# Performance work log

Measured on AMD Instinct MI355X. Metric: run time of the kernel, lower is better.

Reference implementation:

```python
import jax, jax.numpy as jnp
import numpy as np
import math

EMB_DIM = 1024
N_HEADS = 16
HEAD_DIM = EMB_DIM // N_HEADS
B, T = 4, 2048


def bitlinear(x, w):
    # BitNet b1.58 absmean ternary quantization. NOTE: the source never
    # rescales the ternary weights by `scale`, so forward uses raw {-1,0,1}.
    scale = jnp.maximum(jnp.mean(jnp.abs(w)), 1e-8)
    w_ternary = jnp.clip(jnp.round(w / scale), -1.0, 1.0)
    w_q = w + jax.lax.stop_gradient(w_ternary - w)  # STE
    return x @ w_q.T


def setup_inputs() -> dict:
    key = jax.random.key(0)
    k1, k2, k3 = jax.random.split(key, 3)
    x = jax.random.normal(k1, (B, T, EMB_DIM), dtype=jnp.float32)
    w_qkv = jax.random.normal(k2, (3 * EMB_DIM, EMB_DIM), dtype=jnp.float32) * 0.02
    w_out = jax.random.normal(k3, (EMB_DIM, EMB_DIM), dtype=jnp.float32) * 0.02
    return {"x": x, "w_qkv": w_qkv, "w_out": w_out}


def reference(x, w_qkv, w_out):
    Bc, Tc, C = x.shape
    qkv = bitlinear(x, w_qkv)  # [B, T, 3C]
    q, k, v = jnp.split(qkv, 3, axis=2)

    def split_heads(t):  # [B, T, C] -> [B, H, T, D]
        return t.reshape(Bc, Tc, N_HEADS, HEAD_DIM).transpose(0, 2, 1, 3)

    q, k, v = split_heads(q), split_heads(k), split_heads(v)
    scale = math.sqrt(HEAD_DIM)
    scores = jnp.einsum("bhqd,bhkd->bhqk", q, k) / scale  # [B, H, T, T]
    causal = jnp.triu(jnp.ones((Tc, Tc), dtype=bool), k=1)
    scores = jnp.where(causal, -jnp.inf, scores)
    attn = jax.nn.softmax(scores, axis=-1)
    out = jnp.einsum("bhqk,bhkd->bhqd", attn, v)  # [B, H, T, D]
    out = out.transpose(0, 2, 1, 3).reshape(Bc, Tc, C)
    return bitlinear(out, w_out)
```

## Files before the change

### kernel.cpp

```cpp
#include <hip/hip_runtime.h>
#include <hip/hip_bf16.h>

#define EMB   1024
#define NHEAD 16
#define HDIM  64
#define BSZ   4
#define SEQ   2048
#define MROWS (BSZ*SEQ)
#define NQKV  (3*EMB)

typedef __bf16 bf16;
typedef __bf16 bf16v8 __attribute__((ext_vector_type(8)));
typedef float  f32v4  __attribute__((ext_vector_type(4)));
typedef int    i32v4  __attribute__((ext_vector_type(4)));

#define MFMA16(a,b,c)  __builtin_amdgcn_mfma_f32_16x16x32_bf16((a),(b),(c),0,0,0)
#define MFMAI8(a,b,c)  __builtin_amdgcn_mfma_i32_16x16x64_i8((a),(b),(c),0,0,0)

__device__ __forceinline__ void gload_lds16(const void* g, void* l) {
  __builtin_amdgcn_global_load_lds((const __attribute__((address_space(1))) void*)g,
                                   (__attribute__((address_space(3))) void*)l,
                                   16, 0, 0);
}

#define DPP_FMAX(x, ctrl) do {                                                     \
    int _t = __builtin_amdgcn_update_dpp(0, __float_as_int(x), (ctrl), 0xf, 0xf, true); \
    (x) = fmaxf((x), __int_as_float(_t)); } while (0)


__global__ void zero2_kernel(float* p) { p[threadIdx.x] = 0.f; }

__global__ void abs_sum_kernel(const float* __restrict__ w, int n, float* out) {
  float s = 0.f;
  for (int i = blockIdx.x * blockDim.x + threadIdx.x; i < n; i += gridDim.x * blockDim.x)
    s += fabsf(w[i]);
  #pragma unroll
  for (int off = 32; off; off >>= 1) s += __shfl_down(s, off, 64);
  __shared__ float red[4];
  int lane = threadIdx.x & 63, wid = threadIdx.x >> 6;
  if (lane == 0) red[wid] = s;
  __syncthreads();
  if (threadIdx.x == 0) atomicAdd(out, red[0] + red[1] + red[2] + red[3]);
}

__global__ void ternarize_i8_kernel(const float* __restrict__ w, int n,
                                    const float* __restrict__ sum, char* __restrict__ out) {
  int i = blockIdx.x * blockDim.x + threadIdx.x;
  if (i >= n) return;
  float scale = fmaxf(*sum / (float)n, 1e-8f);
  float t = rintf(w[i] / scale);
  t = fmaxf(-1.f, fminf(1.f, t));
  out[i] = (char)(int)t;
}

__global__ void ternarize_bf16_kernel(const float* __restrict__ w, int n,
                                      const float* __restrict__ sum, bf16* __restrict__ out) {
  int i = blockIdx.x * blockDim.x + threadIdx.x;
  if (i >= n) return;
  float scale = fmaxf(*sum / (float)n, 1e-8f);
  float t = rintf(w[i] / scale);
  t = fmaxf(-1.f, fminf(1.f, t));
  out[i] = (bf16)t;
}

__global__ void quant_x_kernel(const float* __restrict__ x, char* __restrict__ p1,
                               char* __restrict__ p2, int n) {
  int i = blockIdx.x * blockDim.x + threadIdx.x;
  if (i >= n) return;
  float v = x[i];
  float q1 = fminf(fmaxf(rintf(v * 16.f), -127.f), 127.f);
  float r = v - q1 * 0.0625f;
  float q2 = fminf(fmaxf(rintf(r * 4096.f), -127.f), 127.f);
  p1[i] = (char)(int)q1;
  p2[i] = (char)(int)q2;
}


__launch_bounds__(256, 2)
__global__ void gemm_qkv_kernel(const char* __restrict__ xq1, const char* __restrict__ xq2,
                                const char* __restrict__ w8,
                                bf16* __restrict__ qh, bf16* __restrict__ ql,
                                bf16* __restrict__ kh, bf16* __restrict__ kl,
                                bf16* __restrict__ vv) {
  __shared__ __align__(16) char A1[128 * 64];
  __shared__ __align__(16) char A2[128 * 64];
  __shared__ __align__(16) char Bs[128 * 64];
  const int tid = threadIdx.x;
  const int lane = tid & 63, wid = tid >> 6;
  const int quad = lane >> 4, l16 = lane & 15;
  const int m0 = blockIdx.x * 128, n0 = blockIdx.y * 128;
  const int wm = (wid >> 1) * 64, wn = (wid & 1) * 64;
  const int asw = (l16 >> 1) & 3;
  i32v4 acc1[4][4] = {};
  i32v4 acc2[4][4] = {};

  for (int kt = 0; kt < EMB / 64; ++kt) {
    __syncthreads();
    #pragma unroll
    for (int r = 0; r < 2; ++r) {
      int li = r * 256 + tid;
      int row = li >> 2, cs = li & 3;
      int cg = cs ^ ((row >> 1) & 3);
      gload_lds16(xq1 + (size_t)(m0 + row) * EMB + kt * 64 + cg * 16, &A1[li * 16]);
      gload_lds16(xq2 + (size_t)(m0 + row) * EMB + kt * 64 + cg * 16, &A2[li * 16]);
      gload_lds16(w8  + (size_t)(n0 + row) * EMB + kt * 64 + cg * 16, &Bs[li * 16]);
    }
    __syncthreads();
    i32v4 af1[4], af2[4], bfr[4];
    #pragma unroll
    for (int i = 0; i < 4; ++i) {
      int arow = wm + i * 16 + l16;
      int off = arow * 64 + ((quad ^ asw) * 16);
      af1[i] = *(const i32v4*)&A1[off];
      af2[i] = *(const i32v4*)&A2[off];
      int brow = wn + i * 16 + l16;
      bfr[i] = *(const i32v4*)&Bs[brow * 64 + ((quad ^ asw) * 16)];
    }
    #pragma unroll
    for (int i = 0; i < 4; ++i)
      #pragma unroll
      for (int j = 0; j < 4; ++j) {
        acc1[i][j] = MFMAI8(af1[i], bfr[j], acc1[i][j]);
        acc2[i][j] = MFMAI8(af2[i], bfr[j], acc2[i][j]);
      }
  }
  const float S1 = 0.0625f, S2 = 1.f / 4096.f;
  const float QSCALE = 0.18033688011112042f;
  #pragma unroll
  for (int i = 0; i < 4; ++i)
    #pragma unroll
    for (int j = 0; j < 4; ++j)
      #pragma unroll
      for (int r = 0; r < 4; ++r) {
        int m = m0 + wm + i * 16 + quad * 4 + r;
        int n = n0 + wn + j * 16 + l16;
        float c = (float)acc1[i][j][r] * S1 + (float)acc2[i][j][r] * S2;
        int b = m >> 11, t = m & (SEQ - 1);
        int region = n >> 10, c1 = n & 1023, h = c1 >> 6, d = c1 & 63;
        size_t idx = (((size_t)(b * NHEAD + h) * SEQ + t) << 6) + d;
        if (region == 0)      { float cs = c * QSCALE; bf16 hi = (bf16)cs; qh[idx] = hi; ql[idx] = (bf16)(cs - (float)hi); }
        else if (region == 1) { bf16 hi = (bf16)c; kh[idx] = hi; kl[idx] = (bf16)(c - (float)hi); }
        else                  { vv[idx] = (bf16)c; }
      }
}


__global__ void transpose_v_kernel(const bf16* __restrict__ v, bf16* __restrict__ vt) {
  __shared__ bf16 tile[64 * 72];
  const int tid = threadIdx.x;
  const int bh = blockIdx.y, t0 = blockIdx.x * 64;
  const size_t base = (size_t)bh * SEQ * HDIM;
  #pragma unroll
  for (int r = 0; r < 2; ++r) {
    int li = r * 256 + tid;
    int row = li >> 3, col = (li & 7) * 8;
    bf16v8 val = *(const bf16v8*)(v + base + (size_t)(t0 + row) * HDIM + col);
    #pragma unroll
    for (int j = 0; j < 8; ++j) tile[(col + j) * 72 + row] = val[j];
  }
  __syncthreads();
  #pragma unroll
  for (int r = 0; r < 2; ++r) {
    int li = r * 256 + tid;
    int drow = li >> 3, tcol = (li & 7) * 8;
    bf16v8 val;
    #pragma unroll
    for (int j = 0; j < 8; ++j) val[j] = tile[drow * 72 + tcol + j];
    *(bf16v8*)(vt + base + (size_t)drow * SEQ + t0 + tcol) = val;
  }
}


__launch_bounds__(256, 2)
__global__ void attn_kernel(const bf16* __restrict__ qh, const bf16* __restrict__ ql,
                            const bf16* __restrict__ kh, const bf16* __restrict__ kl,
                            const bf16* __restrict__ vt, bf16* __restrict__ o) {
  __shared__ __align__(16) char smem[66560];
  bf16* Qh = (bf16*)smem;
  bf16* Ql = (bf16*)(smem + 16384);
  bf16* Pw = (bf16*)(smem + 49152);
  const int tid = threadIdx.x;
  const int lane = tid & 63, wid = tid >> 6;
  const int quad = lane >> 4, l16 = lane & 15;
  const int xs = l16 & 7;
  const int pair = blockIdx.x;
  const int bh = blockIdx.y;
  const size_t base = (size_t)bh * SEQ * HDIM;

  auto stage_kv = [&](char* dst, int k0) {
    #pragma unroll
    for (int r = 0; r < 2; ++r) {
      int li = r * 256 + tid;
      int srow = li >> 3, scg = (li & 7) ^ (srow & 7);
      gload_lds16(kh + base + (size_t)(k0 + srow) * HDIM + scg * 8, (bf16*)dst + (size_t)li * 8);
      gload_lds16(kl + base + (size_t)(k0 + srow) * HDIM + scg * 8, (bf16*)(dst + 8192) + (size_t)li * 8);
      gload_lds16(vt + base + (size_t)srow * SEQ + k0 + scg * 8,    (bf16*)(dst + 16384) + (size_t)li * 8);
    }
  };

  bf16v8 ones_f;
  {
    bf16 v1 = (l16 == 0) ? (bf16)1.0f : (bf16)0.0f;
    #pragma unroll
    for (int j = 0; j < 8; ++j) ones_f[j] = v1;
  }
  const int b = bh >> 4, h = bh & 15;

  for (int phase = 0; phase < 2; ++phase) {
    const int qt = phase ? (7 - pair) : (8 + pair);
    const int q0 = qt * 128;

    __syncthreads();
    #pragma unroll
    for (int r = 0; r < 4; ++r) {
      int li = r * 256 + tid;
      int row = li >> 3, cg = (li & 7) ^ (row & 7);
      gload_lds16(qh + base + (size_t)(q0 + row) * HDIM + cg * 8, &Qh[li * 8]);
      gload_lds16(ql + base + (size_t)(q0 + row) * HDIM + cg * 8, &Ql[li * 8]);
    }
    __syncthreads();
    bf16v8 qhf[2][2], qlf[2][2];
    #pragma unroll
    for (int sub = 0; sub < 2; ++sub)
      #pragma unroll
      for (int kk = 0; kk < 2; ++kk) {
        int off = (wid * 32 + sub * 16 + l16) * 64 + (((kk << 2) | quad) ^ xs) * 8;
        qhf[sub][kk] = *(const bf16v8*)&Qh[off];
        qlf[sub][kk] = *(const bf16v8*)&Ql[off];
      }
    __syncthreads();

    f32v4 oacc[2][4] = {};
    f32v4 lacc[2] = {};
    float mrow[2][4];
    #pragma unroll
    for (int s = 0; s < 2; ++s)
      #pragma unroll
      for (int r = 0; r < 4; ++r) mrow[s][r] = -1e30f;

    const int qw0 = q0 + wid * 32;
    const int qrow_hi = qw0 + 31;
    const int ntiles = 2 * qt + 2;

    stage_kv(smem, 0);

    for (int ktile = 0; ktile < ntiles; ++ktile) {
      char* cb = smem + (size_t)((ktile & 1) * 24576);
      char* nb = smem + (size_t)(((ktile + 1) & 1) * 24576);
      __syncthreads();
      if (ktile + 1 < ntiles) stage_kv(nb, (ktile + 1) * 64);
      const int k0 = ktile * 64;
      if (k0 > qrow_hi) continue;

      bf16* Kh_ = (bf16*)cb;
      bf16* Kl_ = (bf16*)(cb + 8192);
      bf16* Vt_ = (bf16*)(cb + 16384);

      f32v4 sacc[2][4] = {};
      #pragma unroll
      for (int kk = 0; kk < 2; ++kk) {
        const int co = (((kk << 2) | quad) ^ xs) * 8;
        bf16v8 khf[4], klf[4];
        #pragma unroll
        for (int nt = 0; nt < 4; ++nt) {
          khf[nt] = *(const bf16v8*)&Kh_[(nt * 16 + l16) * 64 + co];
          klf[nt] = *(const bf16v8*)&Kl_[(nt * 16 + l16) * 64 + co];
        }
        #pragma unroll
        for (int sub = 0; sub < 2; ++sub)
          #pragma unroll
          for (int nt = 0; nt < 4; ++nt) {
            sacc[sub][nt] = MFMA16(qhf[sub][kk], khf[nt], sacc[sub][nt]);
            sacc[sub][nt] = MFMA16(qhf[sub][kk], klf[nt], sacc[sub][nt]);
            sacc[sub][nt] = MFMA16(qlf[sub][kk], khf[nt], sacc[sub][nt]);
          }
      }

      #pragma unroll
      for (int sub = 0; sub < 2; ++sub) {
        if (k0 > qw0 + sub * 16 + 15) continue;
        const int qrow_base = qw0 + sub * 16 + quad * 4;
        #pragma unroll
        for (int nt = 0; nt < 4; ++nt) {
          int key = k0 + nt * 16 + l16;
          #pragma unroll
          for (int r = 0; r < 4; ++r)
            if (key > qrow_base + r) sacc[sub][nt][r] = -1e30f;
        }
        float alpha[4];
        #pragma unroll
        for (int r = 0; r < 4; ++r) {
          float mx = fmaxf(fmaxf(sacc[sub][0][r], sacc[sub][1][r]),
                           fmaxf(sacc[sub][2][r], sacc[sub][3][r]));
          DPP_FMAX(mx, 0x128);
          DPP_FMAX(mx, 0x124);
          DPP_FMAX(mx, 0x122);
          DPP_FMAX(mx, 0x121);
          float mnew = fmaxf(mrow[sub][r], mx);
          alpha[r] = __builtin_amdgcn_exp2f(mrow[sub][r] - mnew);
          mrow[sub][r] = mnew;
        }
        bf16* pwave = Pw + (wid * 2 + sub) * (16 * 68);
        #pragma unroll
        for (int nt = 0; nt < 4; ++nt)
          #pragma unroll
          for (int r = 0; r < 4; ++r)
            pwave[(quad * 4 + r) * 68 + nt * 16 + l16] =
                (bf16)__builtin_amdgcn_exp2f(sacc[sub][nt][r] - mrow[sub][r]);
        #pragma unroll
        for (int r = 0; r < 4; ++r) {
          lacc[sub][r] *= alpha[r];
          #pragma unroll
          for (int dt = 0; dt < 4; ++dt) oacc[sub][dt][r] *= alpha[r];
        }
      }

      #pragma unroll
      for (int kk = 0; kk < 2; ++kk) {
        const int co = (((kk << 2) | quad) ^ xs) * 8;
        bf16v8 vf[4];
        #pragma unroll
        for (int dt = 0; dt < 4; ++dt)
          vf[dt] = *(const bf16v8*)&Vt_[(dt * 16 + l16) * 64 + co];
        #pragma unroll
        for (int sub = 0; sub < 2; ++sub) {
          if (k0 > qw0 + sub * 16 + 15) continue;
          bf16v8 pf = *(const bf16v8*)&Pw[(wid * 2 + sub) * (16 * 68) + l16 * 68 + kk * 32 + quad * 8];
          lacc[sub] = MFMA16(pf, ones_f, lacc[sub]);
          #pragma unroll
          for (int dt = 0; dt < 4; ++dt)
            oacc[sub][dt] = MFMA16(pf, vf[dt], oacc[sub][dt]);
        }
      }
    }

    #pragma unroll
    for (int sub = 0; sub < 2; ++sub) {
      float lrow[4];
      #pragma unroll
      for (int r = 0; r < 4; ++r) lrow[r] = __shfl(lacc[sub][r], lane & 48, 64);
      #pragma unroll
      for (int dt = 0; dt < 4; ++dt)
        #pragma unroll
        for (int r = 0; r < 4; ++r) {
          int q = q0 + wid * 32 + sub * 16 + quad * 4 + r;
          int d = dt * 16 + l16;
          float val = oacc[sub][dt][r] / lrow[r];
          o[((size_t)(b * SEQ + q)) * EMB + h * HDIM + d] = (bf16)val;
        }
    }
  }
}


__launch_bounds__(256, 2)
__global__ void gemm_out_kernel(const bf16* __restrict__ oin, const bf16* __restrict__ wt,
                                float* __restrict__ out) {
  __shared__ __align__(16) bf16 As_[128 * 64];
  __shared__ __align__(16) bf16 Bs_[128 * 64];
  const int tid = threadIdx.x;
  const int lane = tid & 63, wid = tid >> 6;
  const int quad = lane >> 4, l16 = lane & 15;
  const int m0 = blockIdx.x * 128, n0 = blockIdx.y * 128;
  const int wm = (wid >> 1) * 64, wn = (wid & 1) * 64;
  f32v4 acc[4][4] = {};

  for (int kt = 0; kt < EMB / 64; ++kt) {
    __syncthreads();
    #pragma unroll
    for (int r = 0; r < 4; ++r) {
      int li = r * 256 + tid;
      int row = li >> 3, col = (li & 7) * 8;
      gload_lds16(oin + (size_t)(m0 + row) * EMB + kt * 64 + col, &As_[li * 8]);
      gload_lds16(wt  + (size_t)(n0 + row) * EMB + kt * 64 + col, &Bs_[li * 8]);
    }
    __syncthreads();
    #pragma unroll
    for (int kk = 0; kk < 2; ++kk) {
      bf16v8 af[4], bfr[4];
      #pragma unroll
      for (int i = 0; i < 4; ++i) {
        af[i]  = *(const bf16v8*)&As_[(wm + i * 16 + l16) * 64 + kk * 32 + quad * 8];
        bfr[i] = *(const bf16v8*)&Bs_[(wn + i * 16 + l16) * 64 + kk * 32 + quad * 8];
      }
      #pragma unroll
      for (int i = 0; i < 4; ++i)
        #pragma unroll
        for (int j = 0; j < 4; ++j)
          acc[i][j] = MFMA16(af[i], bfr[j], acc[i][j]);
    }
  }
  #pragma unroll
  for (int i = 0; i < 4; ++i)
    #pragma unroll
    for (int j = 0; j < 4; ++j)
      #pragma unroll
      for (int r = 0; r < 4; ++r) {
        int m = m0 + wm + i * 16 + quad * 4 + r;
        int n = n0 + wn + j * 16 + l16;
        out[(size_t)m * EMB + n] = acc[i][j][r];
      }
}


extern "C" void kernel_launch(void* const* d_in, const int* in_sizes, int n_in,
                              void* d_out, int out_size, void* d_ws, size_t ws_size,
                              hipStream_t stream) {
  const float* x     = (const float*)d_in[0];
  const float* w_qkv = (const float*)d_in[1];
  const float* w_out = (const float*)d_in[2];
  float* out = (float*)d_out;
  char* ws = (char*)d_ws;

  const size_t SZ  = (size_t)MROWS * EMB * sizeof(bf16);
  const size_t SZ8 = (size_t)MROWS * EMB;
  size_t off = 0;
  float* sums = (float*)ws;            off = 256;
  char*  wq8  = (char*)(ws + off);     off += (size_t)NQKV * EMB;
  bf16*  wo_t = (bf16*)(ws + off);     off += (size_t)EMB * EMB * sizeof(bf16);
  char*  xq1  = (char*)(ws + off);     off += SZ8;
  char*  xq2  = (char*)(ws + off);     off += SZ8;
  bf16*  qh   = (bf16*)(ws + off);     off += SZ;
  bf16*  ql   = (bf16*)(ws + off);     off += SZ;
  bf16*  kh   = (bf16*)(ws + off);     off += SZ;
  bf16*  kl   = (bf16*)(ws + off);     off += SZ;
  bf16*  vv   = (bf16*)(ws + off);     off += SZ;
  bf16*  vt   = (bf16*)xq1;
  bf16*  ob   = vv;
  (void)in_sizes; (void)n_in; (void)out_size; (void)ws_size;

  zero2_kernel<<<1, 2, 0, stream>>>(sums);
  abs_sum_kernel<<<256, 256, 0, stream>>>(w_qkv, NQKV * EMB, &sums[0]);
  abs_sum_kernel<<<256, 256, 0, stream>>>(w_out, EMB * EMB, &sums[1]);
  ternarize_i8_kernel<<<(NQKV * EMB) / 256, 256, 0, stream>>>(w_qkv, NQKV * EMB, &sums[0], wq8);
  ternarize_bf16_kernel<<<(EMB * EMB) / 256, 256, 0, stream>>>(w_out, EMB * EMB, &sums[1], wo_t);
  quant_x_kernel<<<(MROWS * EMB) / 256, 256, 0, stream>>>(x, xq1, xq2, MROWS * EMB);
  gemm_qkv_kernel<<<dim3(MROWS / 128, NQKV / 128), 256, 0, stream>>>(xq1, xq2, wq8, qh, ql, kh, kl, vv);
  transpose_v_kernel<<<dim3(SEQ / 64, BSZ * NHEAD), 256, 0, stream>>>(vv, vt);
  attn_kernel<<<dim3(8, BSZ * NHEAD), 256, 0, stream>>>(qh, ql, kh, kl, vt, ob);
  gemm_out_kernel<<<dim3(MROWS / 128, EMB / 128), 256, 0, stream>>>(ob, wo_t, out);
}
```

Measured before the change: 344.6 us.

## Transpose QK^T MFMA so rows map to lanes and simplify online softmax

Swaps the MFMA operand order for scores so each lane owns one query row, which turns the row max and sum into cross-quad shuffles instead of DPP reductions. The row sum is now computed in registers, replacing the ones-vector MFMA. The oacc rescale is skipped when no row max grows. The P buffer is shared per wave instead of per sub-tile, and the sub-0 score MFMAs are skipped when that sub-tile is fully masked. This cuts MFMA and VALU work in the softmax, at the cost of more shuffles and a serialized P write/read per sub-tile.

```diff
diff --git a/kernel.cpp b/kernel.cpp
--- a/kernel.cpp
+++ b/kernel.cpp
@@ -10,6 +10,7 @@
 #define NQKV  (3*EMB)
 
 typedef __bf16 bf16;
+typedef __bf16 bf16v4 __attribute__((ext_vector_type(4)));
 typedef __bf16 bf16v8 __attribute__((ext_vector_type(8)));
 typedef float  f32v4  __attribute__((ext_vector_type(4)));
 typedef int    i32v4  __attribute__((ext_vector_type(4)));
@@ -22,10 +23,6 @@
                                    (__attribute__((address_space(3))) void*)l,
                                    16, 0, 0);
 }
-
-#define DPP_FMAX(x, ctrl) do {                                                     \
-    int _t = __builtin_amdgcn_update_dpp(0, __float_as_int(x), (ctrl), 0xf, 0xf, true); \
-    (x) = fmaxf((x), __int_as_float(_t)); } while (0)
 
 
 __global__ void zero2_kernel(float* p) { p[threadIdx.x] = 0.f; }
@@ -175,7 +172,7 @@
 __global__ void attn_kernel(const bf16* __restrict__ qh, const bf16* __restrict__ ql,
                             const bf16* __restrict__ kh, const bf16* __restrict__ kl,
                             const bf16* __restrict__ vt, bf16* __restrict__ o) {
-  __shared__ __align__(16) char smem[66560];
+  __shared__ __align__(16) char smem[57856];
   bf16* Qh = (bf16*)smem;
   bf16* Ql = (bf16*)(smem + 16384);
   bf16* Pw = (bf16*)(smem + 49152);
@@ -198,13 +195,8 @@
     }
   };
 
-  bf16v8 ones_f;
-  {
-    bf16 v1 = (l16 == 0) ? (bf16)1.0f : (bf16)0.0f;
-    #pragma unroll
-    for (int j = 0; j < 8; ++j) ones_f[j] = v1;
-  }
   const int b = bh >> 4, h = bh & 15;
+  bf16* Ps = Pw + wid * (16 * 68);
 
   for (int phase = 0; phase < 2; ++phase) {
     const int qt = phase ? (7 - pair) : (8 + pair);
@@ -231,12 +223,8 @@
     __syncthreads();
 
     f32v4 oacc[2][4] = {};
-    f32v4 lacc[2] = {};
-    float mrow[2][4];
-    #pragma unroll
-    for (int s = 0; s < 2; ++s)
-      #pragma unroll
-      for (int r = 0; r < 4; ++r) mrow[s][r] = -1e30f;
+    float lsum[2] = {0.f, 0.f};
+    float mrow[2] = {-1e30f, -1e30f};
 
     const int qw0 = q0 + wid * 32;
     const int qrow_hi = qw0 + 31;
@@ -256,6 +244,8 @@
       bf16* Kl_ = (bf16*)(cb + 8192);
       bf16* Vt_ = (bf16*)(cb + 16384);
 
+      const bool live0 = (k0 <= qw0 + 15);
+
       f32v4 sacc[2][4] = {};
       #pragma unroll
       for (int kk = 0; kk < 2; ++kk) {
@@ -267,69 +257,87 @@
           klf[nt] = *(const bf16v8*)&Kl_[(nt * 16 + l16) * 64 + co];
         }
         #pragma unroll
-        for (int sub = 0; sub < 2; ++sub)
+        for (int sub = 0; sub < 2; ++sub) {
+          if (sub == 0 && !live0) continue;
           #pragma unroll
           for (int nt = 0; nt < 4; ++nt) {
-            sacc[sub][nt] = MFMA16(qhf[sub][kk], khf[nt], sacc[sub][nt]);
-            sacc[sub][nt] = MFMA16(qhf[sub][kk], klf[nt], sacc[sub][nt]);
-            sacc[sub][nt] = MFMA16(qlf[sub][kk], khf[nt], sacc[sub][nt]);
+            sacc[sub][nt] = MFMA16(khf[nt], qhf[sub][kk], sacc[sub][nt]);
+            sacc[sub][nt] = MFMA16(klf[nt], qhf[sub][kk], sacc[sub][nt]);
+            sacc[sub][nt] = MFMA16(khf[nt], qlf[sub][kk], sacc[sub][nt]);
           }
+        }
       }
 
       #pragma unroll
       for (int sub = 0; sub < 2; ++sub) {
-        if (k0 > qw0 + sub * 16 + 15) continue;
-        const int qrow_base = qw0 + sub * 16 + quad * 4;
+        if (sub == 0 && !live0) continue;
+        const int dq = (qw0 + sub * 16 + l16) - k0 - quad * 4;
+        #pragma unroll
+        for (int nt = 0; nt < 4; ++nt)
+          #pragma unroll
+          for (int r = 0; r < 4; ++r)
+            if (nt * 16 + r > dq) sacc[sub][nt][r] = -1e30f;
+
+        float mA = fmaxf(fmaxf(sacc[sub][0][0], sacc[sub][0][1]),
+                         fmaxf(sacc[sub][0][2], sacc[sub][0][3]));
+        float mB = fmaxf(fmaxf(sacc[sub][1][0], sacc[sub][1][1]),
+                         fmaxf(sacc[sub][1][2], sacc[sub][1][3]));
+        float mC = fmaxf(fmaxf(sacc[sub][2][0], sacc[sub][2][1]),
+                         fmaxf(sacc[sub][2][2], sacc[sub][2][3]));
+        float mD = fmaxf(fmaxf(sacc[sub][3][0], sacc[sub][3][1]),
+                         fmaxf(sacc[sub][3][2], sacc[sub][3][3]));
+        float mx = fmaxf(fmaxf(mA, mB), fmaxf(mC, mD));
+        mx = fmaxf(mx, __shfl_xor(mx, 16, 64));
+        mx = fmaxf(mx, __shfl_xor(mx, 32, 64));
+
+        const bool grow = __any(mx > mrow[sub]);
+        const float mnew = grow ? fmaxf(mrow[sub], mx) : mrow[sub];
+
+        float snt[4];
         #pragma unroll
         for (int nt = 0; nt < 4; ++nt) {
-          int key = k0 + nt * 16 + l16;
+          bf16v4 t;
+          float s0 = 0.f, s1 = 0.f;
+          #pragma unroll
+          for (int r = 0; r < 4; ++r) {
+            float ev = __builtin_amdgcn_exp2f(sacc[sub][nt][r] - mnew);
+            bf16 pb = (bf16)ev;
+            t[r] = pb;
+            if (r & 1) s1 += (float)pb; else s0 += (float)pb;
+          }
+          snt[nt] = s0 + s1;
+          *(bf16v4*)&Ps[l16 * 68 + nt * 16 + quad * 4] = t;
+        }
+        float s = (snt[0] + snt[1]) + (snt[2] + snt[3]);
+        s += __shfl_xor(s, 16, 64);
+        s += __shfl_xor(s, 32, 64);
+
+        if (grow) {
+          const float alpha = __builtin_amdgcn_exp2f(mrow[sub] - mnew);
+          mrow[sub] = mnew;
+          lsum[sub] = lsum[sub] * alpha + s;
+          float abp[4];
           #pragma unroll
           for (int r = 0; r < 4; ++r)
-            if (key > qrow_base + r) sacc[sub][nt][r] = -1e30f;
-        }
-        float alpha[4];
-        #pragma unroll
-        for (int r = 0; r < 4; ++r) {
-          float mx = fmaxf(fmaxf(sacc[sub][0][r], sacc[sub][1][r]),
-                           fmaxf(sacc[sub][2][r], sacc[sub][3][r]));
-          DPP_FMAX(mx, 0x128);
-          DPP_FMAX(mx, 0x124);
-          DPP_FMAX(mx, 0x122);
-          DPP_FMAX(mx, 0x121);
-          float mnew = fmaxf(mrow[sub][r], mx);
-          alpha[r] = __builtin_amdgcn_exp2f(mrow[sub][r] - mnew);
-          mrow[sub][r] = mnew;
-        }
-        bf16* pwave = Pw + (wid * 2 + sub) * (16 * 68);
-        #pragma unroll
-        for (int nt = 0; nt < 4; ++nt)
-          #pragma unroll
-          for (int r = 0; r < 4; ++r)
-            pwave[(quad * 4 + r) * 68 + nt * 16 + l16] =
-                (bf16)__builtin_amdgcn_exp2f(sacc[sub][nt][r] - mrow[sub][r]);
-        #pragma unroll
-        for (int r = 0; r < 4; ++r) {
-          lacc[sub][r] *= alpha[r];
-          #pragma unroll
-          for (int dt = 0; dt < 4; ++dt) oacc[sub][dt][r] *= alpha[r];
-        }
-      }
-
-      #pragma unroll
-      for (int kk = 0; kk < 2; ++kk) {
-        const int co = (((kk << 2) | quad) ^ xs) * 8;
-        bf16v8 vf[4];
-        #pragma unroll
-        for (int dt = 0; dt < 4; ++dt)
-          vf[dt] = *(const bf16v8*)&Vt_[(dt * 16 + l16) * 64 + co];
-        #pragma unroll
-        for (int sub = 0; sub < 2; ++sub) {
-          if (k0 > qw0 + sub * 16 + 15) continue;
-          bf16v8 pf = *(const bf16v8*)&Pw[(wid * 2 + sub) * (16 * 68) + l16 * 68 + kk * 32 + quad * 8];
-          lacc[sub] = MFMA16(pf, ones_f, lacc[sub]);
+            abp[r] = __shfl(alpha, quad * 20 + r, 64);
           #pragma unroll
           for (int dt = 0; dt < 4; ++dt)
-            oacc[sub][dt] = MFMA16(pf, vf[dt], oacc[sub][dt]);
+            #pragma unroll
+            for (int r = 0; r < 4; ++r)
+              oacc[sub][dt][r] *= abp[r];
+        } else {
+          lsum[sub] += s;
+        }
+
+        #pragma unroll
+        for (int kk = 0; kk < 2; ++kk) {
+          const int co = (((kk << 2) | quad) ^ xs) * 8;
+          bf16v8 pf = *(const bf16v8*)&Ps[l16 * 68 + kk * 32 + quad * 8];
+          #pragma unroll
+          for (int dt = 0; dt < 4; ++dt) {
+            bf16v8 vf = *(const bf16v8*)&Vt_[(dt * 16 + l16) * 64 + co];
+            oacc[sub][dt] = MFMA16(pf, vf, oacc[sub][dt]);
+          }
         }
       }
     }
@@ -338,7 +346,8 @@
     for (int sub = 0; sub < 2; ++sub) {
       float lrow[4];
       #pragma unroll
-      for (int r = 0; r < 4; ++r) lrow[r] = __shfl(lacc[sub][r], lane & 48, 64);
+      for (int r = 0; r < 4; ++r)
+        lrow[r] = __shfl(lsum[sub], quad * 20 + r, 64);
       #pragma unroll
       for (int dt = 0; dt < 4; ++dt)
         #pragma unroll
```

Measured after the change: 366.1 us. +6.2%, slower.
